# Kernel tuning notes

Measured on AMD Instinct MI355X. Metric: run time of the kernel, lower is better.

The kernel has to match this reference:

```python
import jax, jax.numpy as jnp
import numpy as np
from jax import lax

B, C, H, W = 8, 64, 256, 256
WSIZES = [8, 8]
DRATES = [1, 2]
SHIFT = True
CS = C // len(WSIZES)          # split channels = 32
SCALE = CS ** (-0.5)
EPS = 1e-6


def _ln2d(x, w, b):
    # channel-wise LayerNorm over dim 1 (biased variance), per LayerNormFunction
    mu = x.mean(1, keepdims=True)
    var = ((x - mu) ** 2).mean(1, keepdims=True)
    y = (x - mu) / jnp.sqrt(var + EPS)
    return w[None, :, None, None] * y + b[None, :, None, None]


def _conv1d(x, w, pad, dil):
    # x: [b, ci, L], w: [co, ci, k]
    return lax.conv_general_dilated(x, w, (1,), ((pad, pad),), rhs_dilation=(dil,),
                                    dimension_numbers=('NCH', 'OIH', 'NCH'))


def _eca(x, w1, w2, w3, wc):
    # x: [b,c,h,w] -> channel attention [b,c,1,1]
    y = x.mean((2, 3))[:, None, :]                      # [b,1,c]
    y1 = _conv1d(y, w1, 1, 1)
    y2 = _conv1d(y, w2, 2, 2)
    y3 = _conv1d(y, w3, 4, 4)
    y = _conv1d(jnp.concatenate([y1, y2, y3], axis=1), wc, 1, 1)  # [b,1,c]
    return jax.nn.sigmoid(jnp.transpose(y, (0, 2, 1))[..., None])  # [b,c,1,1]


def _conv1x1(x, w):
    # w: [co, ci]
    return jnp.einsum('bchw,oc->bohw', x, w)


def _win(x, ws):
    # [b,c,H,W] -> [(b nh nw), ws*ws, c]
    b, c, h, w = x.shape
    nh, nw = h // ws, w // ws
    x = x.reshape(b, c, nh, ws, nw, ws).transpose(0, 2, 4, 3, 5, 1)
    return x.reshape(b * nh * nw, ws * ws, c)


def _unwin(x, b, nh, nw, ws):
    c = x.shape[-1]
    x = x.reshape(b, nh, nw, ws, ws, c).transpose(0, 5, 1, 3, 2, 4)
    return x.reshape(b, c, nh * ws, nw * ws)


def setup_inputs() -> dict:
    key = jax.random.key(0)
    ks = jax.random.split(key, 16)
    g = lambda k, shape: jax.random.normal(k, shape, jnp.float32) * 0.02
    return {
        'x0': jax.random.normal(ks[0], (B, C, H, W), jnp.float32),
        'ln_w': jnp.ones((C,), jnp.float32),
        'ln_b': jnp.zeros((C,), jnp.float32),
        'dw_w': g(ks[1], (C, 1, 3, 3)),
        'dw_b': jnp.zeros((C,), jnp.float32),
        'eca_w1': g(ks[2], (1, 1, 3)),
        'eca_w2': g(ks[3], (1, 1, 3)),
        'eca_w3': g(ks[4], (1, 1, 3)),
        'eca_wc': g(ks[5], (1, 3, 3)),
        'wq': g(ks[6], (C, C)),
        'wk': g(ks[7], (C, C)),
        'wv': g(ks[8], (C, C)),
        'down_w': g(ks[9], (CS, 1, 2, 2)),
        'down_b': jnp.zeros((CS,), jnp.float32),
        'sa_w': g(ks[10], (1, C)),
        'sa_b': jnp.zeros((1,), jnp.float32),
        'po_w': g(ks[11], (C, C)),
        'po_b': jnp.zeros((C,), jnp.float32),
    }


def reference(x0, ln_w, ln_b, dw_w, dw_b, eca_w1, eca_w2, eca_w3, eca_wc,
              wq, wk, wv, down_w, down_b, sa_w, sa_b, po_w, po_b):
    b, c, h, w = x0.shape
    x = _ln2d(x0, ln_w, ln_b)
    # depthwise 3x3
    x1 = lax.conv_general_dilated(x, dw_w, (1, 1), ((1, 1), (1, 1)),
                                  feature_group_count=c,
                                  dimension_numbers=('NCHW', 'OIHW', 'NCHW'))
    x1 = x1 + dw_b[None, :, None, None]
    ca = _eca(x1, eca_w1, eca_w2, eca_w3, eca_wc)
    vs = jnp.split(_conv1x1(x, wv) * ca, len(WSIZES), axis=1)
    qs = jnp.split(_conv1x1(x, wq), len(WSIZES), axis=1)
    ks_ = jnp.split(_conv1x1(x, wk), len(WSIZES), axis=1)

    ys = []
    for idx in range(len(WSIZES)):
        ws = WSIZES[idx]
        ds = ws // DRATES[idx]
        q = qs[idx]
        if SHIFT:
            q = jnp.roll(q, (-ws // 2, -ws // 2), (2, 3))
        q = _win(q, ws)
        if DRATES[idx] != 1:
            # depthwise 2x2 stride-2 downsample of k, v
            def down(t):
                t = lax.conv_general_dilated(t, down_w, (2, 2), 'VALID',
                                             feature_group_count=CS,
                                             dimension_numbers=('NCHW', 'OIHW', 'NCHW'))
                return t + down_b[None, :, None, None]
            k = down(ks_[idx])
            v = down(vs[idx])
            if SHIFT:
                k = jnp.roll(k, (-ds // 2, -ds // 2), (2, 3))
                v = jnp.roll(v, (-ds // 2, -ds // 2), (2, 3))
            k = _win(k, ds)
            v = _win(v, ds)
        else:
            k, v = ks_[idx], vs[idx]
            if SHIFT:
                k = jnp.roll(k, (-ws // 2, -ws // 2), (2, 3))
                v = jnp.roll(v, (-ws // 2, -ws // 2), (2, 3))
            k = _win(k, ws)
            v = _win(v, ws)
        atn = jax.nn.softmax(jnp.einsum('nqc,nkc->nqk', q, k) * SCALE, axis=-1)
        y_ = jnp.einsum('nqk,nkc->nqc', atn, v)
        y_ = _unwin(y_, b, h // ws, w // ws, ws)
        if SHIFT:
            y_ = jnp.roll(y_, (ws // 2, ws // 2), (2, 3))
        ys.append(y_)

    y = jnp.concatenate(ys, axis=1)
    x1m = jax.nn.sigmoid(_conv1x1(y, sa_w) + sa_b[None, :, None, None]) * x1
    y = _conv1x1(y + x1m, po_w) + po_b[None, :, None, None]
    return y + x0
```

## Files before the change

### kernel.cpp

```cpp
#include <hip/hip_runtime.h>
#include <hip/hip_bf16.h>

using bf16 = __hip_bfloat16;

constexpr int B = 8, C = 64, H = 256, W = 256;
constexpr int HWs = H * W;
constexpr int NPIX = B * H * W;
constexpr long long NELEM = (long long)B * C * H * W;
constexpr int CS = 32;
constexpr int Hd = 128, Wd = 128;
constexpr int HWd = Hd * Wd;
constexpr int NDOWN = B * CS * HWd;
constexpr float EPS = 1e-6f;
constexpr float SCALE = 0.17677669529663687f;

typedef __attribute__((ext_vector_type(8))) short short8v;
typedef __attribute__((ext_vector_type(8))) unsigned short ushort8v;
typedef __attribute__((ext_vector_type(4))) unsigned short ushort4v;
typedef __attribute__((ext_vector_type(4))) float f32x4;

__device__ __forceinline__ float b2f(bf16 v) { return __bfloat162float(v); }
__device__ __forceinline__ bf16 f2b(float v) { return __float2bfloat16(v); }
__device__ __forceinline__ unsigned short f2bu(float v) {
  bf16 t = __float2bfloat16(v);
  unsigned short u;
  __builtin_memcpy(&u, &t, 2);
  return u;
}
__device__ __forceinline__ float bu2f(unsigned short u) {
  bf16 t;
  __builtin_memcpy(&t, &u, 2);
  return __bfloat162float(t);
}
__device__ __forceinline__ short8v pack2(ushort4v a, ushort4v b) {
  short8v r;
  r[0] = (short)a[0]; r[1] = (short)a[1]; r[2] = (short)a[2]; r[3] = (short)a[3];
  r[4] = (short)b[0]; r[5] = (short)b[1]; r[6] = (short)b[2]; r[7] = (short)b[3];
  return r;
}

__global__ __launch_bounds__(256) void ln_kernel(
    const float* __restrict__ x0, const float* __restrict__ lw,
    const float* __restrict__ lb, bf16* __restrict__ xo) {
  int p = blockIdx.x * 256 + threadIdx.x;
  int b = p >> 16, hw = p & (HWs - 1);
  const float* xp = x0 + (size_t)b * C * HWs + hw;
  float xv[C];
  float s = 0.f;
#pragma unroll
  for (int c = 0; c < C; ++c) { xv[c] = xp[(size_t)c * HWs]; s += xv[c]; }
  float mu = s * (1.f / C);
  float vs = 0.f;
#pragma unroll
  for (int c = 0; c < C; ++c) { float d = xv[c] - mu; vs += d * d; }
  float rstd = rsqrtf(vs * (1.f / C) + EPS);
  bf16* yp = xo + (size_t)b * C * HWs + hw;
#pragma unroll
  for (int c = 0; c < C; ++c)
    yp[(size_t)c * HWs] = f2b(lw[c] * ((xv[c] - mu) * rstd) + lb[c]);
}

__global__ __launch_bounds__(256) void dw_kernel(
    const unsigned short* __restrict__ x, const float* __restrict__ dww,
    const float* __restrict__ dwb, unsigned short* __restrict__ x1,
    float* __restrict__ pool) {
  int tid = threadIdx.x;
  int tx = tid & 15, ty = tid >> 4;
  int h = blockIdx.x * 16 + ty;
  int c = blockIdx.y, b = blockIdx.z;
  const unsigned short* xp = x + ((size_t)b * C + c) * HWs;
  float kk[9];
#pragma unroll
  for (int i = 0; i < 9; ++i) kk[i] = dww[c * 9 + i];
  int w0 = tx * 16;
  float acc[16];
  float bias = dwb[c];
#pragma unroll
  for (int i = 0; i < 16; ++i) acc[i] = bias;
#pragma unroll
  for (int dr = 0; dr < 3; ++dr) {
    int hh = h + dr - 1;
    if (hh < 0 || hh >= H) continue;
    const unsigned short* rp = xp + hh * W;
    ushort8v r0 = *(const ushort8v*)(rp + w0);
    ushort8v r1 = *(const ushort8v*)(rp + w0 + 8);
    float p[18];
    p[0] = (w0 > 0) ? bu2f(rp[w0 - 1]) : 0.f;
    p[17] = (w0 + 16 < W) ? bu2f(rp[w0 + 16]) : 0.f;
#pragma unroll
    for (int i = 0; i < 8; ++i) { p[1 + i] = bu2f(r0[i]); p[9 + i] = bu2f(r1[i]); }
    float k0 = kk[dr * 3], k1 = kk[dr * 3 + 1], k2 = kk[dr * 3 + 2];
#pragma unroll
    for (int i = 0; i < 16; ++i)
      acc[i] += k0 * p[i] + k1 * p[i + 1] + k2 * p[i + 2];
  }
  ushort8v o0, o1;
  float s = 0.f;
#pragma unroll
  for (int i = 0; i < 8; ++i) { o0[i] = f2bu(acc[i]); o1[i] = f2bu(acc[i + 8]); }
#pragma unroll
  for (int i = 0; i < 16; ++i) s += acc[i];
  size_t ob = ((size_t)b * C + c) * HWs + h * W + w0;
  *(ushort8v*)(x1 + ob) = o0;
  *(ushort8v*)(x1 + ob + 8) = o1;
#pragma unroll
  for (int off = 32; off > 0; off >>= 1) s += __shfl_down(s, off, 64);
  __shared__ float red[4];
  if ((tid & 63) == 0) red[tid >> 6] = s;
  __syncthreads();
  if (tid == 0) atomicAdd(&pool[b * C + c], red[0] + red[1] + red[2] + red[3]);
}

__global__ __launch_bounds__(512) void eca_kernel(
    const float* __restrict__ pool, const float* __restrict__ w1,
    const float* __restrict__ w2, const float* __restrict__ w3,
    const float* __restrict__ wc, float* __restrict__ ca) {
  int tid = threadIdx.x;
  int b = tid >> 6, c = tid & 63;
  __shared__ float m[8][64], t1[8][64], t2[8][64], t3[8][64];
  m[b][c] = pool[tid] * (1.f / HWs);
  __syncthreads();
  auto gm = [&](int cc) -> float { return (cc >= 0 && cc < 64) ? m[b][cc] : 0.f; };
  t1[b][c] = w1[0] * gm(c - 1) + w1[1] * gm(c) + w1[2] * gm(c + 1);
  t2[b][c] = w2[0] * gm(c - 2) + w2[1] * gm(c) + w2[2] * gm(c + 2);
  t3[b][c] = w3[0] * gm(c - 4) + w3[1] * gm(c) + w3[2] * gm(c + 4);
  __syncthreads();
  auto g1 = [&](int cc) -> float { return (cc >= 0 && cc < 64) ? t1[b][cc] : 0.f; };
  auto g2 = [&](int cc) -> float { return (cc >= 0 && cc < 64) ? t2[b][cc] : 0.f; };
  auto g3 = [&](int cc) -> float { return (cc >= 0 && cc < 64) ? t3[b][cc] : 0.f; };
  float z = 0.f;
#pragma unroll
  for (int k = 0; k < 3; ++k) {
    z += wc[0 * 3 + k] * g1(c + k - 1);
    z += wc[1 * 3 + k] * g2(c + k - 1);
    z += wc[2 * 3 + k] * g3(c + k - 1);
  }
  ca[tid] = 1.f / (1.f + __expf(-z));
}

__global__ __launch_bounds__(256) void qkv_mfma_kernel(
    const unsigned short* __restrict__ x, const float* __restrict__ wq,
    const float* __restrict__ wk, const float* __restrict__ wv,
    const float* __restrict__ ca, unsigned short* __restrict__ q0,
    unsigned short* __restrict__ q1, unsigned short* __restrict__ k0,
    unsigned short* __restrict__ v0, unsigned short* __restrict__ ksp,
    unsigned short* __restrict__ vsp) {
  int lane = threadIdx.x & 63, wid = threadIdx.x >> 6;
  int lr = lane & 15, lg = lane >> 4;
  short8v aq[4][2], ak[4][2], av[4][2];
#pragma unroll
  for (int mt = 0; mt < 4; ++mt)
#pragma unroll
    for (int ks = 0; ks < 2; ++ks) {
      int rowoff = (mt * 16 + lr) * 64 + ks * 32 + lg * 4;
      short8v tq, tk, tv;
#pragma unroll
      for (int j = 0; j < 8; ++j) {
        int kj = (j & 3) + 16 * (j >> 2);
        tq[j] = (short)f2bu(wq[rowoff + kj]);
        tk[j] = (short)f2bu(wk[rowoff + kj]);
        tv[j] = (short)f2bu(wv[rowoff + kj]);
      }
      aq[mt][ks] = tq; ak[mt][ks] = tk; av[mt][ks] = tv;
    }
  const int NT = NPIX / 16;
  for (int t = blockIdx.x * 4 + wid; t < NT; t += gridDim.x * 4) {
    int p0 = t * 16;
    int b = p0 >> 16;
    int hw0 = p0 & (HWs - 1);
    const unsigned short* xp = x + (size_t)b * C * HWs + hw0 + lr;
    short8v bx[2];
#pragma unroll
    for (int ks = 0; ks < 2; ++ks) {
      short8v tt;
#pragma unroll
      for (int j = 0; j < 8; ++j) {
        int c = ks * 32 + lg * 4 + (j & 3) + 16 * (j >> 2);
        tt[j] = (short)xp[(size_t)c * HWs];
      }
      bx[ks] = tt;
    }
    f32x4 zero = {0.f, 0.f, 0.f, 0.f};
    f32x4 acq[4], ack[4], acv[4];
#pragma unroll
    for (int mt = 0; mt < 4; ++mt) {
      acq[mt] = __builtin_amdgcn_mfma_f32_16x16x32_bf16(aq[mt][0], bx[0], zero, 0, 0, 0);
      acq[mt] = __builtin_amdgcn_mfma_f32_16x16x32_bf16(aq[mt][1], bx[1], acq[mt], 0, 0, 0);
      ack[mt] = __builtin_amdgcn_mfma_f32_16x16x32_bf16(ak[mt][0], bx[0], zero, 0, 0, 0);
      ack[mt] = __builtin_amdgcn_mfma_f32_16x16x32_bf16(ak[mt][1], bx[1], ack[mt], 0, 0, 0);
      acv[mt] = __builtin_amdgcn_mfma_f32_16x16x32_bf16(av[mt][0], bx[0], zero, 0, 0, 0);
      acv[mt] = __builtin_amdgcn_mfma_f32_16x16x32_bf16(av[mt][1], bx[1], acv[mt], 0, 0, 0);
    }
    int r = hw0 >> 8;
    int cpix = (hw0 & 255) + lr;
    int rr = (r - 4) & 255, cc = (cpix - 4) & 255;
    int windex = b * 1024 + (rr >> 3) * 32 + (cc >> 3);
    int tok = (rr & 7) * 8 + (cc & 7);
    size_t wbase = (size_t)windex * 2048 + (size_t)tok * 32;
    const float* cab = ca + b * 64;
#pragma unroll
    for (int mt = 0; mt < 4; ++mt) {
      int och = mt * 16 + lg * 4;
      ushort4v hq, hk, hv;
#pragma unroll
      for (int i = 0; i < 4; ++i) {
        hq[i] = f2bu(acq[mt][i]);
        hk[i] = f2bu(ack[mt][i]);
        hv[i] = f2bu(acv[mt][i] * cab[och + i]);
      }
      if (mt < 2) {
        *(ushort4v*)(q0 + wbase + och) = hq;
        *(ushort4v*)(k0 + wbase + och) = hk;
        *(ushort4v*)(v0 + wbase + och) = hv;
      } else {
        *(ushort4v*)(q1 + wbase + (och - 32)) = hq;
        size_t sb = ((size_t)b * 32 + (och - 32)) * HWs + hw0 + lr;
#pragma unroll
        for (int i = 0; i < 4; ++i) {
          ksp[sb + (size_t)i * HWs] = hk[i];
          vsp[sb + (size_t)i * HWs] = hv[i];
        }
      }
    }
  }
}

__global__ __launch_bounds__(256) void down_kernel(
    const unsigned short* __restrict__ ksp, const unsigned short* __restrict__ vsp,
    const float* __restrict__ dw, const float* __restrict__ db,
    unsigned short* __restrict__ kdw, unsigned short* __restrict__ vdw) {
  int t = blockIdx.x * 256 + threadIdx.x;
  int wxd = t & 31, i = (t >> 5) & 127, c = (t >> 12) & 31, b = t >> 17;
  const unsigned short* kp = ksp + ((size_t)b * 32 + c) * HWs;
  const unsigned short* vp = vsp + ((size_t)b * 32 + c) * HWs;
  float w00 = dw[c * 4], w01 = dw[c * 4 + 1], w10 = dw[c * 4 + 2], w11 = dw[c * 4 + 3];
  float bias = db[c];
  int rowa = (2 * i) * W, rowb = rowa + W;
  int rr = (i - 2) & 127;
  size_t winb = ((size_t)(b * 1024 + (rr >> 2) * 32 + wxd)) * 512;
  int tokrow = (rr & 3) * 4;
  ushort4v hk, hv;
#pragma unroll
  for (int tx = 0; tx < 4; ++tx) {
    int j = (wxd * 4 + tx + 2) & 127;
    int c0 = 2 * j;
    float ka = w00 * bu2f(kp[rowa + c0]) + w01 * bu2f(kp[rowa + c0 + 1]) +
               w10 * bu2f(kp[rowb + c0]) + w11 * bu2f(kp[rowb + c0 + 1]) + bias;
    float va = w00 * bu2f(vp[rowa + c0]) + w01 * bu2f(vp[rowa + c0 + 1]) +
               w10 * bu2f(vp[rowb + c0]) + w11 * bu2f(vp[rowb + c0 + 1]) + bias;
    hk[tx] = f2bu(ka);
    hv[tx] = f2bu(va);
  }
  *(ushort4v*)(vdw + winb + (size_t)c * 16 + tokrow) = hv;
#pragma unroll
  for (int tx = 0; tx < 4; ++tx)
    kdw[winb + (size_t)(tokrow + tx) * 32 + c] = hk[tx];
}

__global__ __launch_bounds__(256) void attn0_kernel(
    const unsigned short* __restrict__ q0, const unsigned short* __restrict__ k0,
    const unsigned short* __restrict__ v0, unsigned short* __restrict__ y) {
  __shared__ unsigned short zs[4][32][72];
  int lane = threadIdx.x & 63, wid = threadIdx.x >> 6;
  int lr = lane & 15, lg = lane >> 4;
  int widx = blockIdx.x * 4 + wid;
  int b = widx >> 10, wy = (widx >> 5) & 31, wx = widx & 31;
  unsigned short* zw = &zs[wid][0][0];
  {
    const unsigned short* vp = v0 + (size_t)widx * 2048 + (size_t)lane * 32;
#pragma unroll
    for (int j2 = 0; j2 < 4; ++j2) {
      ushort8v vv = *(const ushort8v*)(vp + j2 * 8);
#pragma unroll
      for (int i = 0; i < 8; ++i) zw[(j2 * 8 + i) * 72 + lane] = vv[i];
    }
  }
  const unsigned short* kw = k0 + (size_t)widx * 2048;
  const unsigned short* qw = q0 + (size_t)widx * 2048;
  short8v kf[4], qf[4];
#pragma unroll
  for (int kt = 0; kt < 4; ++kt) {
    ushort4v a = *(const ushort4v*)(kw + (kt * 16 + lr) * 32 + lg * 4);
    ushort4v b2 = *(const ushort4v*)(kw + (kt * 16 + lr) * 32 + lg * 4 + 16);
    kf[kt] = pack2(a, b2);
  }
#pragma unroll
  for (int qt = 0; qt < 4; ++qt) {
    ushort4v a = *(const ushort4v*)(qw + (qt * 16 + lr) * 32 + lg * 4);
    ushort4v b2 = *(const ushort4v*)(qw + (qt * 16 + lr) * 32 + lg * 4 + 16);
    qf[qt] = pack2(a, b2);
  }
  __syncthreads();
  short8v va[2][2];
#pragma unroll
  for (int mt = 0; mt < 2; ++mt)
#pragma unroll
    for (int ck = 0; ck < 2; ++ck) {
      ushort4v a = *(const ushort4v*)&zw[(mt * 16 + lr) * 72 + ck * 32 + lg * 4];
      ushort4v b2 = *(const ushort4v*)&zw[(mt * 16 + lr) * 72 + ck * 32 + lg * 4 + 16];
      va[mt][ck] = pack2(a, b2);
    }
  f32x4 zero = {0.f, 0.f, 0.f, 0.f};
#pragma unroll
  for (int qt = 0; qt < 4; ++qt) {
    f32x4 st[4];
#pragma unroll
    for (int kt = 0; kt < 4; ++kt)
      st[kt] = __builtin_amdgcn_mfma_f32_16x16x32_bf16(kf[kt], qf[qt], zero, 0, 0, 0);
    float mx = -1e30f;
#pragma unroll
    for (int kt = 0; kt < 4; ++kt)
#pragma unroll
      for (int r2 = 0; r2 < 4; ++r2) mx = fmaxf(mx, st[kt][r2]);
    mx = fmaxf(mx, __shfl_xor(mx, 16, 64));
    mx = fmaxf(mx, __shfl_xor(mx, 32, 64));
    float sum = 0.f;
#pragma unroll
    for (int kt = 0; kt < 4; ++kt)
#pragma unroll
      for (int r2 = 0; r2 < 4; ++r2) {
        float e = __expf(SCALE * (st[kt][r2] - mx));
        st[kt][r2] = e;
        sum += e;
      }
    sum += __shfl_xor(sum, 16, 64);
    sum += __shfl_xor(sum, 32, 64);
    float inv = 1.f / sum;
    short8v pb[2];
#pragma unroll
    for (int ck = 0; ck < 2; ++ck)
#pragma unroll
      for (int j = 0; j < 8; ++j)
        pb[ck][j] = (short)f2bu(st[ck * 2 + (j >> 2)][j & 3]);
#pragma unroll
    for (int mt = 0; mt < 2; ++mt) {
      f32x4 yt = __builtin_amdgcn_mfma_f32_16x16x32_bf16(va[mt][0], pb[0], zero, 0, 0, 0);
      yt = __builtin_amdgcn_mfma_f32_16x16x32_bf16(va[mt][1], pb[1], yt, 0, 0, 0);
#pragma unroll
      for (int r2 = 0; r2 < 4; ++r2)
        zw[(mt * 16 + lg * 4 + r2) * 72 + qt * 16 + lr] = f2bu(yt[r2] * inv);
    }
  }
  __syncthreads();
  int ch = lane & 31, rh = lane >> 5;
  size_t ybase = ((size_t)b * C + ch) * HWs;
  int c1 = wx * 8 + 4, c2 = (wx * 8 + 8) & 255;
#pragma unroll
  for (int k2 = 0; k2 < 4; ++k2) {
    int row = rh * 4 + k2;
    ushort8v t8 = *(const ushort8v*)&zw[ch * 72 + row * 8];
    int r = (wy * 8 + row + 4) & 255;
    ushort4v lo, hi;
#pragma unroll
    for (int i = 0; i < 4; ++i) { lo[i] = t8[i]; hi[i] = t8[4 + i]; }
    *(ushort4v*)(y + ybase + r * W + c1) = lo;
    *(ushort4v*)(y + ybase + r * W + c2) = hi;
  }
}

__global__ __launch_bounds__(256) void attn1_kernel(
    const unsigned short* __restrict__ q1, const unsigned short* __restrict__ kdw,
    const unsigned short* __restrict__ vdw, unsigned short* __restrict__ y) {
  __shared__ unsigned short zs[4][32][72];
  int lane = threadIdx.x & 63, wid = threadIdx.x >> 6;
  int lr = lane & 15, lg = lane >> 4;
  int widx = blockIdx.x * 4 + wid;
  int b = widx >> 10, wy = (widx >> 5) & 31, wx = widx & 31;
  unsigned short* zw = &zs[wid][0][0];
  short8v kfr;
  {
    ushort4v a = *(const ushort4v*)(kdw + (size_t)widx * 512 + lr * 32 + lg * 4);
    ushort4v b2 = *(const ushort4v*)(kdw + (size_t)widx * 512 + lr * 32 + lg * 4 + 16);
    kfr = pack2(a, b2);
  }
  short8v va[2];
#pragma unroll
  for (int mt = 0; mt < 2; ++mt) {
    ushort4v a = *(const ushort4v*)(vdw + (size_t)widx * 512 + (mt * 16 + lr) * 16 + lg * 4);
    short8v t;
#pragma unroll
    for (int i = 0; i < 4; ++i) { t[i] = (short)a[i]; t[4 + i] = 0; }
    va[mt] = t;
  }
  const unsigned short* qw = q1 + (size_t)widx * 2048;
  short8v qf[4];
#pragma unroll
  for (int qt = 0; qt < 4; ++qt) {
    ushort4v a = *(const ushort4v*)(qw + (qt * 16 + lr) * 32 + lg * 4);
    ushort4v b2 = *(const ushort4v*)(qw + (qt * 16 + lr) * 32 + lg * 4 + 16);
    qf[qt] = pack2(a, b2);
  }
  f32x4 zero = {0.f, 0.f, 0.f, 0.f};
#pragma unroll
  for (int qt = 0; qt < 4; ++qt) {
    f32x4 st = __builtin_amdgcn_mfma_f32_16x16x32_bf16(kfr, qf[qt], zero, 0, 0, 0);
    float mx = fmaxf(fmaxf(st[0], st[1]), fmaxf(st[2], st[3]));
    mx = fmaxf(mx, __shfl_xor(mx, 16, 64));
    mx = fmaxf(mx, __shfl_xor(mx, 32, 64));
    float sum = 0.f;
#pragma unroll
    for (int r2 = 0; r2 < 4; ++r2) {
      float e = __expf(SCALE * (st[r2] - mx));
      st[r2] = e;
      sum += e;
    }
    sum += __shfl_xor(sum, 16, 64);
    sum += __shfl_xor(sum, 32, 64);
    float inv = 1.f / sum;
    short8v pb;
#pragma unroll
    for (int j = 0; j < 4; ++j) { pb[j] = (short)f2bu(st[j]); pb[4 + j] = 0; }
#pragma unroll
    for (int mt = 0; mt < 2; ++mt) {
      f32x4 yt = __builtin_amdgcn_mfma_f32_16x16x32_bf16(va[mt], pb, zero, 0, 0, 0);
#pragma unroll
      for (int r2 = 0; r2 < 4; ++r2)
        zw[(mt * 16 + lg * 4 + r2) * 72 + qt * 16 + lr] = f2bu(yt[r2] * inv);
    }
  }
  __syncthreads();
  int ch = lane & 31, rh = lane >> 5;
  size_t ybase = ((size_t)b * C + 32 + ch) * HWs;
  int c1 = wx * 8 + 4, c2 = (wx * 8 + 8) & 255;
#pragma unroll
  for (int k2 = 0; k2 < 4; ++k2) {
    int row = rh * 4 + k2;
    ushort8v t8 = *(const ushort8v*)&zw[ch * 72 + row * 8];
    int r = (wy * 8 + row + 4) & 255;
    ushort4v lo, hi;
#pragma unroll
    for (int i = 0; i < 4; ++i) { lo[i] = t8[i]; hi[i] = t8[4 + i]; }
    *(ushort4v*)(y + ybase + r * W + c1) = lo;
    *(ushort4v*)(y + ybase + r * W + c2) = hi;
  }
}

__global__ __launch_bounds__(256) void final_mfma_kernel(
    const unsigned short* __restrict__ y, const unsigned short* __restrict__ x1,
    const float* __restrict__ x0, const float* __restrict__ sa_w,
    const float* __restrict__ sa_b, const float* __restrict__ po_w,
    const float* __restrict__ po_b, float* __restrict__ out) {
  __shared__ unsigned short zs[64][72];
  __shared__ float part[4][64];
  __shared__ float sgs[64];
  int tid = threadIdx.x;
  int lane = tid & 63, wid = tid >> 6;
  int lr = lane & 15, lg = lane >> 4;
  short8v ap[4][2];
#pragma unroll
  for (int mt = 0; mt < 4; ++mt)
#pragma unroll
    for (int ks = 0; ks < 2; ++ks) {
      int rowoff = (mt * 16 + lr) * 64 + ks * 32 + lg * 4;
      short8v tt;
#pragma unroll
      for (int j = 0; j < 8; ++j) {
        int kj = (j & 3) + 16 * (j >> 2);
        tt[j] = (short)f2bu(po_w[rowoff + kj]);
      }
      ap[mt][ks] = tt;
    }
  int cc = tid >> 2, qx = (tid & 3) * 16;
  const int NBLK = NPIX / 64;
  for (int blk = blockIdx.x; blk < NBLK; blk += gridDim.x) {
    int p0 = blk * 64;
    int b = p0 >> 16, hw0 = p0 & (HWs - 1);
    size_t rbase = (size_t)b * C * HWs + (size_t)cc * HWs + hw0 + qx;
    ushort8v y0 = *(const ushort8v*)(y + rbase);
    ushort8v y1 = *(const ushort8v*)(y + rbase + 8);
    ushort8v a0 = *(const ushort8v*)(x1 + rbase);
    ushort8v a1 = *(const ushort8v*)(x1 + rbase + 8);
    *(ushort8v*)&zs[cc][qx] = y0;
    *(ushort8v*)&zs[cc][qx + 8] = y1;
    __syncthreads();
    {
      int p = tid & 63, qr = tid >> 6;
      float s = 0.f;
#pragma unroll
      for (int c2 = 0; c2 < 16; ++c2)
        s += sa_w[qr * 16 + c2] * bu2f(zs[qr * 16 + c2][p]);
      part[qr][p] = s;
    }
    __syncthreads();
    if (tid < 64) {
      float sd = part[0][tid] + part[1][tid] + part[2][tid] + part[3][tid] + sa_b[0];
      sgs[tid] = 1.f / (1.f + __expf(-sd));
    }
    __syncthreads();
    {
      ushort8v z0, z1;
#pragma unroll
      for (int i = 0; i < 8; ++i) {
        z0[i] = f2bu(bu2f(y0[i]) + sgs[qx + i] * bu2f(a0[i]));
        z1[i] = f2bu(bu2f(y1[i]) + sgs[qx + 8 + i] * bu2f(a1[i]));
      }
      *(ushort8v*)&zs[cc][qx] = z0;
      *(ushort8v*)&zs[cc][qx + 8] = z1;
    }
    __syncthreads();
    short8v bz[2];
#pragma unroll
    for (int ks = 0; ks < 2; ++ks) {
      short8v tt;
#pragma unroll
      for (int j = 0; j < 8; ++j) {
        int c2 = ks * 32 + lg * 4 + (j & 3) + 16 * (j >> 2);
        tt[j] = (short)zs[c2][wid * 16 + lr];
      }
      bz[ks] = tt;
    }
    f32x4 zero = {0.f, 0.f, 0.f, 0.f};
    f32x4 acc[4];
#pragma unroll
    for (int mt = 0; mt < 4; ++mt) {
      acc[mt] = __builtin_amdgcn_mfma_f32_16x16x32_bf16(ap[mt][0], bz[0], zero, 0, 0, 0);
      acc[mt] = __builtin_amdgcn_mfma_f32_16x16x32_bf16(ap[mt][1], bz[1], acc[mt], 0, 0, 0);
    }
    size_t pbase = (size_t)b * C * HWs + hw0 + wid * 16 + lr;
#pragma unroll
    for (int mt = 0; mt < 4; ++mt)
#pragma unroll
      for (int i = 0; i < 4; ++i) {
        int o = mt * 16 + lg * 4 + i;
        out[pbase + (size_t)o * HWs] = acc[mt][i] + po_b[o] + x0[pbase + (size_t)o * HWs];
      }
    __syncthreads();
  }
}

extern "C" void kernel_launch(void* const* d_in, const int* in_sizes, int n_in,
                              void* d_out, int out_size, void* d_ws, size_t ws_size,
                              hipStream_t stream) {
  const float* x0    = (const float*)d_in[0];
  const float* ln_w  = (const float*)d_in[1];
  const float* ln_b  = (const float*)d_in[2];
  const float* dw_w  = (const float*)d_in[3];
  const float* dw_b  = (const float*)d_in[4];
  const float* ew1   = (const float*)d_in[5];
  const float* ew2   = (const float*)d_in[6];
  const float* ew3   = (const float*)d_in[7];
  const float* ewc   = (const float*)d_in[8];
  const float* wq    = (const float*)d_in[9];
  const float* wk    = (const float*)d_in[10];
  const float* wv    = (const float*)d_in[11];
  const float* dwn_w = (const float*)d_in[12];
  const float* dwn_b = (const float*)d_in[13];
  const float* sa_w  = (const float*)d_in[14];
  const float* sa_b  = (const float*)d_in[15];
  const float* po_w  = (const float*)d_in[16];
  const float* po_b  = (const float*)d_in[17];
  float* out = (float*)d_out;

  char* ws = (char*)d_ws;
  const size_t NB = (size_t)NELEM * sizeof(bf16);
  const size_t NH = NB / 2;
  const size_t NDB = (size_t)NDOWN * sizeof(bf16);
  bf16* xbuf  = (bf16*)(ws);
  bf16* x1buf = (bf16*)(ws + NB);
  unsigned short* q0b  = (unsigned short*)(ws + 2 * NB);
  unsigned short* q1b  = (unsigned short*)(ws + 2 * NB + NH);
  unsigned short* k0b  = (unsigned short*)(ws + 3 * NB);
  unsigned short* v0b  = (unsigned short*)(ws + 3 * NB + NH);
  unsigned short* kspb = (unsigned short*)(ws + 4 * NB);
  unsigned short* vspb = (unsigned short*)(ws + 4 * NB + NH);
  unsigned short* kdwb = (unsigned short*)(ws + 5 * NB);
  unsigned short* vdwb = (unsigned short*)(ws + 5 * NB + NDB);
  float* pool = (float*)(ws + 5 * NB + 2 * NDB);
  float* cabuf = pool + B * C;
  bf16* ybuf = xbuf;

  hipMemsetAsync(pool, 0, B * C * sizeof(float), stream);
  ln_kernel<<<NPIX / 256, 256, 0, stream>>>(x0, ln_w, ln_b, xbuf);
  dw_kernel<<<dim3(16, C, B), 256, 0, stream>>>((const unsigned short*)xbuf, dw_w, dw_b,
                                                (unsigned short*)x1buf, pool);
  eca_kernel<<<1, 512, 0, stream>>>(pool, ew1, ew2, ew3, ewc, cabuf);
  qkv_mfma_kernel<<<2048, 256, 0, stream>>>((const unsigned short*)xbuf, wq, wk, wv,
                                            cabuf, q0b, q1b, k0b, v0b, kspb, vspb);
  down_kernel<<<4096, 256, 0, stream>>>(kspb, vspb, dwn_w, dwn_b, kdwb, vdwb);
  attn0_kernel<<<2048, 256, 0, stream>>>(q0b, k0b, v0b, (unsigned short*)ybuf);
  attn1_kernel<<<2048, 256, 0, stream>>>(q1b, kdwb, vdwb, (unsigned short*)ybuf);
  final_mfma_kernel<<<2048, 256, 0, stream>>>((const unsigned short*)ybuf,
                                              (const unsigned short*)x1buf, x0,
                                              sa_w, sa_b, po_w, po_b, out);
}
```

Measured before the change: 401.9 us.

## Fuse LayerNorm into QKV projection and move channel attention scale into attention

LayerNorm is merged into the QKV MFMA kernel, so x0 is read once and the normalized x is written from the same pass, removing a separate kernel and a bf16 re-read. QKV outputs are staged through LDS so global stores become wide 16-byte stores instead of 4-element scattered ones. The ECA channel scale on V is moved out of the projection and applied to the attention outputs, which lets QKV run before the ECA pool is computed. This relies on softmax rows summing to one and changes bf16 rounding order. The down kernel also switches to vectorized 4-wide loads.

```diff
diff --git a/kernel.cpp b/kernel.cpp
--- a/kernel.cpp
+++ b/kernel.cpp
@@ -39,25 +39,165 @@
   return r;
 }
 
-__global__ __launch_bounds__(256) void ln_kernel(
-    const float* __restrict__ x0, const float* __restrict__ lw,
-    const float* __restrict__ lb, bf16* __restrict__ xo) {
-  int p = blockIdx.x * 256 + threadIdx.x;
-  int b = p >> 16, hw = p & (HWs - 1);
-  const float* xp = x0 + (size_t)b * C * HWs + hw;
-  float xv[C];
-  float s = 0.f;
-#pragma unroll
-  for (int c = 0; c < C; ++c) { xv[c] = xp[(size_t)c * HWs]; s += xv[c]; }
-  float mu = s * (1.f / C);
-  float vs = 0.f;
-#pragma unroll
-  for (int c = 0; c < C; ++c) { float d = xv[c] - mu; vs += d * d; }
-  float rstd = rsqrtf(vs * (1.f / C) + EPS);
-  bf16* yp = xo + (size_t)b * C * HWs + hw;
-#pragma unroll
-  for (int c = 0; c < C; ++c)
-    yp[(size_t)c * HWs] = f2b(lw[c] * ((xv[c] - mu) * rstd) + lb[c]);
+__global__ __launch_bounds__(256) void qkv_ln_kernel(
+    const float* __restrict__ x0, const float* __restrict__ lnw,
+    const float* __restrict__ lnb, const float* __restrict__ wq,
+    const float* __restrict__ wk, const float* __restrict__ wv,
+    unsigned short* __restrict__ xo, unsigned short* __restrict__ q0,
+    unsigned short* __restrict__ q1, unsigned short* __restrict__ k0,
+    unsigned short* __restrict__ v0, unsigned short* __restrict__ ksp,
+    unsigned short* __restrict__ vsp) {
+  __shared__ unsigned short zs[4][4][16 * 80];
+  int lane = threadIdx.x & 63, wid = threadIdx.x >> 6;
+  int lr = lane & 15, lg = lane >> 4;
+  short8v aq[4][2], ak[4][2], av[4][2];
+#pragma unroll
+  for (int mt = 0; mt < 4; ++mt)
+#pragma unroll
+    for (int ks = 0; ks < 2; ++ks) {
+      int rowoff = (mt * 16 + lr) * 64 + ks * 32 + lg * 4;
+      short8v tq, tk, tv;
+#pragma unroll
+      for (int j = 0; j < 8; ++j) {
+        int kj = (j & 3) + 16 * (j >> 2);
+        tq[j] = (short)f2bu(wq[rowoff + kj]);
+        tk[j] = (short)f2bu(wk[rowoff + kj]);
+        tv[j] = (short)f2bu(wv[rowoff + kj]);
+      }
+      aq[mt][ks] = tq; ak[mt][ks] = tk; av[mt][ks] = tv;
+    }
+  float lwv[16], lbv[16];
+#pragma unroll
+  for (int ks = 0; ks < 2; ++ks)
+#pragma unroll
+    for (int j = 0; j < 8; ++j) {
+      int c = ks * 32 + lg * 4 + (j & 3) + 16 * (j >> 2);
+      lwv[ks * 8 + j] = lnw[c];
+      lbv[ks * 8 + j] = lnb[c];
+    }
+  unsigned short* zq = &zs[wid][0][0];
+  unsigned short* zk = &zs[wid][1][0];
+  unsigned short* zv = &zs[wid][2][0];
+  unsigned short* zx = &zs[wid][3][0];
+  const int NT = NPIX / 16;
+  for (int t = blockIdx.x * 4 + wid; t < NT; t += gridDim.x * 4) {
+    int p0 = t * 16;
+    int b = p0 >> 16;
+    int hw0 = p0 & (HWs - 1);
+    const float* xp = x0 + (size_t)b * C * HWs + hw0 + lr;
+    float xv[16];
+#pragma unroll
+    for (int ks = 0; ks < 2; ++ks)
+#pragma unroll
+      for (int j = 0; j < 8; ++j) {
+        int c = ks * 32 + lg * 4 + (j & 3) + 16 * (j >> 2);
+        xv[ks * 8 + j] = xp[(size_t)c * HWs];
+      }
+    float s = 0.f, s2 = 0.f;
+#pragma unroll
+    for (int i = 0; i < 16; ++i) { s += xv[i]; s2 += xv[i] * xv[i]; }
+    s += __shfl_xor(s, 16, 64); s += __shfl_xor(s, 32, 64);
+    s2 += __shfl_xor(s2, 16, 64); s2 += __shfl_xor(s2, 32, 64);
+    float mu = s * (1.f / 64);
+    float var = s2 * (1.f / 64) - mu * mu;
+    float rstd = rsqrtf(var + EPS);
+    short8v bx[2];
+#pragma unroll
+    for (int ks = 0; ks < 2; ++ks)
+#pragma unroll
+      for (int j = 0; j < 8; ++j) {
+        float xn = lwv[ks * 8 + j] * ((xv[ks * 8 + j] - mu) * rstd) + lbv[ks * 8 + j];
+        bx[ks][j] = (short)f2bu(xn);
+      }
+#pragma unroll
+    for (int ks = 0; ks < 2; ++ks)
+#pragma unroll
+      for (int j = 0; j < 8; ++j) {
+        int c = ks * 32 + lg * 4 + (j & 3) + 16 * (j >> 2);
+        zx[lr * 80 + c] = (unsigned short)bx[ks][j];
+      }
+    f32x4 zero = {0.f, 0.f, 0.f, 0.f};
+    {
+      f32x4 acc[4];
+#pragma unroll
+      for (int mt = 0; mt < 4; ++mt) {
+        acc[mt] = __builtin_amdgcn_mfma_f32_16x16x32_bf16(aq[mt][0], bx[0], zero, 0, 0, 0);
+        acc[mt] = __builtin_amdgcn_mfma_f32_16x16x32_bf16(aq[mt][1], bx[1], acc[mt], 0, 0, 0);
+      }
+#pragma unroll
+      for (int mt = 0; mt < 4; ++mt)
+#pragma unroll
+        for (int i = 0; i < 4; ++i)
+          zq[lr * 80 + mt * 16 + lg * 4 + i] = f2bu(acc[mt][i]);
+    }
+    {
+      f32x4 acc[4];
+#pragma unroll
+      for (int mt = 0; mt < 4; ++mt) {
+        acc[mt] = __builtin_amdgcn_mfma_f32_16x16x32_bf16(ak[mt][0], bx[0], zero, 0, 0, 0);
+        acc[mt] = __builtin_amdgcn_mfma_f32_16x16x32_bf16(ak[mt][1], bx[1], acc[mt], 0, 0, 0);
+      }
+#pragma unroll
+      for (int mt = 0; mt < 4; ++mt)
+#pragma unroll
+        for (int i = 0; i < 4; ++i)
+          zk[lr * 80 + mt * 16 + lg * 4 + i] = f2bu(acc[mt][i]);
+    }
+    {
+      f32x4 acc[4];
+#pragma unroll
+      for (int mt = 0; mt < 4; ++mt) {
+        acc[mt] = __builtin_amdgcn_mfma_f32_16x16x32_bf16(av[mt][0], bx[0], zero, 0, 0, 0);
+        acc[mt] = __builtin_amdgcn_mfma_f32_16x16x32_bf16(av[mt][1], bx[1], acc[mt], 0, 0, 0);
+      }
+#pragma unroll
+      for (int mt = 0; mt < 4; ++mt)
+#pragma unroll
+        for (int i = 0; i < 4; ++i)
+          zv[lr * 80 + mt * 16 + lg * 4 + i] = f2bu(acc[mt][i]);
+    }
+    int r = hw0 >> 8, col0 = hw0 & 255;
+    int rr = (r - 4) & 255;
+    int tokr = (rr & 7) * 8;
+    int wrow = b * 1024 + (rr >> 3) * 32;
+    {
+      int px = lane & 15, ch4 = lane >> 4;
+      int cc = (col0 + px - 4) & 255;
+      size_t wb = (size_t)(wrow + (cc >> 3)) * 2048 + (size_t)(tokr + (cc & 7)) * 32 + ch4 * 8;
+      ushort8v dq0 = *(const ushort8v*)&zq[px * 80 + ch4 * 8];
+      ushort8v dq1 = *(const ushort8v*)&zq[px * 80 + 32 + ch4 * 8];
+      ushort8v dk = *(const ushort8v*)&zk[px * 80 + ch4 * 8];
+      ushort8v dv = *(const ushort8v*)&zv[px * 80 + ch4 * 8];
+      *(ushort8v*)(q0 + wb) = dq0;
+      *(ushort8v*)(q1 + wb) = dq1;
+      *(ushort8v*)(k0 + wb) = dk;
+      *(ushort8v*)(v0 + wb) = dv;
+    }
+    {
+      int ch = 32 + (lane & 31), ph = lane >> 5;
+      ushort8v dk, dv;
+#pragma unroll
+      for (int j2 = 0; j2 < 8; ++j2) {
+        dk[j2] = zk[(ph * 8 + j2) * 80 + ch];
+        dv[j2] = zv[(ph * 8 + j2) * 80 + ch];
+      }
+      size_t sb = ((size_t)b * 32 + (ch - 32)) * HWs + hw0 + ph * 8;
+      *(ushort8v*)(ksp + sb) = dk;
+      *(ushort8v*)(vsp + sb) = dv;
+    }
+    {
+      int ch = lane;
+      ushort8v d0, d1;
+#pragma unroll
+      for (int j2 = 0; j2 < 8; ++j2) {
+        d0[j2] = zx[j2 * 80 + ch];
+        d1[j2] = zx[(8 + j2) * 80 + ch];
+      }
+      size_t sb = ((size_t)b * 64 + ch) * HWs + hw0;
+      *(ushort8v*)(xo + sb) = d0;
+      *(ushort8v*)(xo + sb + 8) = d1;
+    }
+  }
 }
 
 __global__ __launch_bounds__(256) void dw_kernel(
@@ -138,93 +278,6 @@
   ca[tid] = 1.f / (1.f + __expf(-z));
 }
 
-__global__ __launch_bounds__(256) void qkv_mfma_kernel(
-    const unsigned short* __restrict__ x, const float* __restrict__ wq,
-    const float* __restrict__ wk, const float* __restrict__ wv,
-    const float* __restrict__ ca, unsigned short* __restrict__ q0,
-    unsigned short* __restrict__ q1, unsigned short* __restrict__ k0,
-    unsigned short* __restrict__ v0, unsigned short* __restrict__ ksp,
-    unsigned short* __restrict__ vsp) {
-  int lane = threadIdx.x & 63, wid = threadIdx.x >> 6;
-  int lr = lane & 15, lg = lane >> 4;
-  short8v aq[4][2], ak[4][2], av[4][2];
-#pragma unroll
-  for (int mt = 0; mt < 4; ++mt)
-#pragma unroll
-    for (int ks = 0; ks < 2; ++ks) {
-      int rowoff = (mt * 16 + lr) * 64 + ks * 32 + lg * 4;
-      short8v tq, tk, tv;
-#pragma unroll
-      for (int j = 0; j < 8; ++j) {
-        int kj = (j & 3) + 16 * (j >> 2);
-        tq[j] = (short)f2bu(wq[rowoff + kj]);
-        tk[j] = (short)f2bu(wk[rowoff + kj]);
-        tv[j] = (short)f2bu(wv[rowoff + kj]);
-      }
-      aq[mt][ks] = tq; ak[mt][ks] = tk; av[mt][ks] = tv;
-    }
-  const int NT = NPIX / 16;
-  for (int t = blockIdx.x * 4 + wid; t < NT; t += gridDim.x * 4) {
-    int p0 = t * 16;
-    int b = p0 >> 16;
-    int hw0 = p0 & (HWs - 1);
-    const unsigned short* xp = x + (size_t)b * C * HWs + hw0 + lr;
-    short8v bx[2];
-#pragma unroll
-    for (int ks = 0; ks < 2; ++ks) {
-      short8v tt;
-#pragma unroll
-      for (int j = 0; j < 8; ++j) {
-        int c = ks * 32 + lg * 4 + (j & 3) + 16 * (j >> 2);
-        tt[j] = (short)xp[(size_t)c * HWs];
-      }
-      bx[ks] = tt;
-    }
-    f32x4 zero = {0.f, 0.f, 0.f, 0.f};
-    f32x4 acq[4], ack[4], acv[4];
-#pragma unroll
-    for (int mt = 0; mt < 4; ++mt) {
-      acq[mt] = __builtin_amdgcn_mfma_f32_16x16x32_bf16(aq[mt][0], bx[0], zero, 0, 0, 0);
-      acq[mt] = __builtin_amdgcn_mfma_f32_16x16x32_bf16(aq[mt][1], bx[1], acq[mt], 0, 0, 0);
-      ack[mt] = __builtin_amdgcn_mfma_f32_16x16x32_bf16(ak[mt][0], bx[0], zero, 0, 0, 0);
-      ack[mt] = __builtin_amdgcn_mfma_f32_16x16x32_bf16(ak[mt][1], bx[1], ack[mt], 0, 0, 0);
-      acv[mt] = __builtin_amdgcn_mfma_f32_16x16x32_bf16(av[mt][0], bx[0], zero, 0, 0, 0);
-      acv[mt] = __builtin_amdgcn_mfma_f32_16x16x32_bf16(av[mt][1], bx[1], acv[mt], 0, 0, 0);
-    }
-    int r = hw0 >> 8;
-    int cpix = (hw0 & 255) + lr;
-    int rr = (r - 4) & 255, cc = (cpix - 4) & 255;
-    int windex = b * 1024 + (rr >> 3) * 32 + (cc >> 3);
-    int tok = (rr & 7) * 8 + (cc & 7);
-    size_t wbase = (size_t)windex * 2048 + (size_t)tok * 32;
-    const float* cab = ca + b * 64;
-#pragma unroll
-    for (int mt = 0; mt < 4; ++mt) {
-      int och = mt * 16 + lg * 4;
-      ushort4v hq, hk, hv;
-#pragma unroll
-      for (int i = 0; i < 4; ++i) {
-        hq[i] = f2bu(acq[mt][i]);
-        hk[i] = f2bu(ack[mt][i]);
-        hv[i] = f2bu(acv[mt][i] * cab[och + i]);
-      }
-      if (mt < 2) {
-        *(ushort4v*)(q0 + wbase + och) = hq;
-        *(ushort4v*)(k0 + wbase + och) = hk;
-        *(ushort4v*)(v0 + wbase + och) = hv;
-      } else {
-        *(ushort4v*)(q1 + wbase + (och - 32)) = hq;
-        size_t sb = ((size_t)b * 32 + (och - 32)) * HWs + hw0 + lr;
-#pragma unroll
-        for (int i = 0; i < 4; ++i) {
-          ksp[sb + (size_t)i * HWs] = hk[i];
-          vsp[sb + (size_t)i * HWs] = hv[i];
-        }
-      }
-    }
-  }
-}
-
 __global__ __launch_bounds__(256) void down_kernel(
     const unsigned short* __restrict__ ksp, const unsigned short* __restrict__ vsp,
     const float* __restrict__ dw, const float* __restrict__ db,
@@ -236,20 +289,35 @@
   float w00 = dw[c * 4], w01 = dw[c * 4 + 1], w10 = dw[c * 4 + 2], w11 = dw[c * 4 + 3];
   float bias = db[c];
   int rowa = (2 * i) * W, rowb = rowa + W;
+  int c0a = (8 * wxd + 4) & 255, c0b = (8 * wxd + 8) & 255;
+  ushort4v ka0 = *(const ushort4v*)(kp + rowa + c0a);
+  ushort4v ka1 = *(const ushort4v*)(kp + rowa + c0b);
+  ushort4v kb0 = *(const ushort4v*)(kp + rowb + c0a);
+  ushort4v kb1 = *(const ushort4v*)(kp + rowb + c0b);
+  ushort4v va0 = *(const ushort4v*)(vp + rowa + c0a);
+  ushort4v va1 = *(const ushort4v*)(vp + rowa + c0b);
+  ushort4v vb0 = *(const ushort4v*)(vp + rowb + c0a);
+  ushort4v vb1 = *(const ushort4v*)(vp + rowb + c0b);
   int rr = (i - 2) & 127;
   size_t winb = ((size_t)(b * 1024 + (rr >> 2) * 32 + wxd)) * 512;
   int tokrow = (rr & 3) * 4;
   ushort4v hk, hv;
 #pragma unroll
   for (int tx = 0; tx < 4; ++tx) {
-    int j = (wxd * 4 + tx + 2) & 127;
-    int c0 = 2 * j;
-    float ka = w00 * bu2f(kp[rowa + c0]) + w01 * bu2f(kp[rowa + c0 + 1]) +
-               w10 * bu2f(kp[rowb + c0]) + w11 * bu2f(kp[rowb + c0 + 1]) + bias;
-    float va = w00 * bu2f(vp[rowa + c0]) + w01 * bu2f(vp[rowa + c0 + 1]) +
-               w10 * bu2f(vp[rowb + c0]) + w11 * bu2f(vp[rowb + c0 + 1]) + bias;
-    hk[tx] = f2bu(ka);
-    hv[tx] = f2bu(va);
+    float k00, k01, k10, k11, v00, v01, v10, v11;
+    if (tx < 2) {
+      k00 = bu2f(ka0[2 * tx]); k01 = bu2f(ka0[2 * tx + 1]);
+      k10 = bu2f(kb0[2 * tx]); k11 = bu2f(kb0[2 * tx + 1]);
+      v00 = bu2f(va0[2 * tx]); v01 = bu2f(va0[2 * tx + 1]);
+      v10 = bu2f(vb0[2 * tx]); v11 = bu2f(vb0[2 * tx + 1]);
+    } else {
+      k00 = bu2f(ka1[2 * (tx - 2)]); k01 = bu2f(ka1[2 * (tx - 2) + 1]);
+      k10 = bu2f(kb1[2 * (tx - 2)]); k11 = bu2f(kb1[2 * (tx - 2) + 1]);
+      v00 = bu2f(va1[2 * (tx - 2)]); v01 = bu2f(va1[2 * (tx - 2) + 1]);
+      v10 = bu2f(vb1[2 * (tx - 2)]); v11 = bu2f(vb1[2 * (tx - 2) + 1]);
+    }
+    hk[tx] = f2bu(w00 * k00 + w01 * k01 + w10 * k10 + w11 * k11 + bias);
+    hv[tx] = f2bu(w00 * v00 + w01 * v01 + w10 * v10 + w11 * v11 + bias);
   }
   *(ushort4v*)(vdw + winb + (size_t)c * 16 + tokrow) = hv;
 #pragma unroll
@@ -259,13 +327,20 @@
 
 __global__ __launch_bounds__(256) void attn0_kernel(
     const unsigned short* __restrict__ q0, const unsigned short* __restrict__ k0,
-    const unsigned short* __restrict__ v0, unsigned short* __restrict__ y) {
+    const unsigned short* __restrict__ v0, const float* __restrict__ ca,
+    unsigned short* __restrict__ y) {
   __shared__ unsigned short zs[4][32][72];
   int lane = threadIdx.x & 63, wid = threadIdx.x >> 6;
   int lr = lane & 15, lg = lane >> 4;
   int widx = blockIdx.x * 4 + wid;
   int b = widx >> 10, wy = (widx >> 5) & 31, wx = widx & 31;
   unsigned short* zw = &zs[wid][0][0];
+  float cav[8];
+#pragma unroll
+  for (int mt = 0; mt < 2; ++mt)
+#pragma unroll
+    for (int r2 = 0; r2 < 4; ++r2)
+      cav[mt * 4 + r2] = ca[b * 64 + mt * 16 + lg * 4 + r2];
   {
     const unsigned short* vp = v0 + (size_t)widx * 2048 + (size_t)lane * 32;
 #pragma unroll
@@ -338,7 +413,7 @@
       yt = __builtin_amdgcn_mfma_f32_16x16x32_bf16(va[mt][1], pb[1], yt, 0, 0, 0);
 #pragma unroll
       for (int r2 = 0; r2 < 4; ++r2)
-        zw[(mt * 16 + lg * 4 + r2) * 72 + qt * 16 + lr] = f2bu(yt[r2] * inv);
+        zw[(mt * 16 + lg * 4 + r2) * 72 + qt * 16 + lr] = f2bu(yt[r2] * inv * cav[mt * 4 + r2]);
     }
   }
   __syncthreads();
@@ -360,13 +435,20 @@
 
 __global__ __launch_bounds__(256) void attn1_kernel(
     const unsigned short* __restrict__ q1, const unsigned short* __restrict__ kdw,
-    const unsigned short* __restrict__ vdw, unsigned short* __restrict__ y) {
+    const unsigned short* __restrict__ vdw, const float* __restrict__ ca,
+    unsigned short* __restrict__ y) {
   __shared__ unsigned short zs[4][32][72];
   int lane = threadIdx.x & 63, wid = threadIdx.x >> 6;
   int lr = lane & 15, lg = lane >> 4;
   int widx = blockIdx.x * 4 + wid;
   int b = widx >> 10, wy = (widx >> 5) & 31, wx = widx & 31;
   unsigned short* zw = &zs[wid][0][0];
+  float cav[8];
+#pragma unroll
+  for (int mt = 0; mt < 2; ++mt)
+#pragma unroll
+    for (int r2 = 0; r2 < 4; ++r2)
+      cav[mt * 4 + r2] = ca[b * 64 + 32 + mt * 16 + lg * 4 + r2];
   short8v kfr;
   {
     ushort4v a = *(const ushort4v*)(kdw + (size_t)widx * 512 + lr * 32 + lg * 4);
@@ -415,7 +497,7 @@
       f32x4 yt = __builtin_amdgcn_mfma_f32_16x16x32_bf16(va[mt], pb, zero, 0, 0, 0);
 #pragma unroll
       for (int r2 = 0; r2 < 4; ++r2)
-        zw[(mt * 16 + lg * 4 + r2) * 72 + qt * 16 + lr] = f2bu(yt[r2] * inv);
+        zw[(mt * 16 + lg * 4 + r2) * 72 + qt * 16 + lr] = f2bu(yt[r2] * inv * cav[mt * 4 + r2]);
     }
   }
   __syncthreads();
@@ -570,15 +652,15 @@
   bf16* ybuf = xbuf;
 
   hipMemsetAsync(pool, 0, B * C * sizeof(float), stream);
-  ln_kernel<<<NPIX / 256, 256, 0, stream>>>(x0, ln_w, ln_b, xbuf);
+  qkv_ln_kernel<<<2048, 256, 0, stream>>>(x0, ln_w, ln_b, wq, wk, wv,
+                                          (unsigned short*)xbuf, q0b, q1b, k0b, v0b,
+                                          kspb, vspb);
   dw_kernel<<<dim3(16, C, B), 256, 0, stream>>>((const unsigned short*)xbuf, dw_w, dw_b,
                                                 (unsigned short*)x1buf, pool);
   eca_kernel<<<1, 512, 0, stream>>>(pool, ew1, ew2, ew3, ewc, cabuf);
-  qkv_mfma_kernel<<<2048, 256, 0, stream>>>((const unsigned short*)xbuf, wq, wk, wv,
-                                            cabuf, q0b, q1b, k0b, v0b, kspb, vspb);
   down_kernel<<<4096, 256, 0, stream>>>(kspb, vspb, dwn_w, dwn_b, kdwb, vdwb);
-  attn0_kernel<<<2048, 256, 0, stream>>>(q0b, k0b, v0b, (unsigned short*)ybuf);
-  attn1_kernel<<<2048, 256, 0, stream>>>(q1b, kdwb, vdwb, (unsigned short*)ybuf);
+  attn0_kernel<<<2048, 256, 0, stream>>>(q0b, k0b, v0b, cabuf, (unsigned short*)ybuf);
+  attn1_kernel<<<2048, 256, 0, stream>>>(q1b, kdwb, vdwb, cabuf, (unsigned short*)ybuf);
   final_mfma_kernel<<<2048, 256, 0, stream>>>((const unsigned short*)ybuf,
                                               (const unsigned short*)x1buf, x0,
                                               sa_w, sa_b, po_w, po_b, out);
```

Measured after the change: 410.6 us (median of 2 runs). 1.02x slower.
